# Performance work log

Hardware: AMD Instinct MI355X
Metric: run time of the kernel (lower is better)

## Reference

```python
import jax, jax.numpy as jnp
import numpy as np

D_MODEL = 1024
N_EXPERTS = 8
TOP_K = 2


def setup_inputs() -> dict:
    key = jax.random.key(0)
    ks = jax.random.split(key, 8)
    B, S, D, E, H = 4, 2048, D_MODEL, N_EXPERTS, 4 * D_MODEL
    s1 = 1.0 / np.sqrt(D)
    s2 = 1.0 / np.sqrt(H)
    return {
        "x": jax.random.normal(ks[0], (B, S, D), dtype=jnp.float32),
        "Wg": jax.random.uniform(ks[1], (D, E), jnp.float32, -s1, s1),
        "bg": jax.random.uniform(ks[2], (E,), jnp.float32, -s1, s1),
        "W1": jax.random.uniform(ks[3], (E, D, H), jnp.float32, -s1, s1),
        "b1": jax.random.uniform(ks[4], (E, H), jnp.float32, -s1, s1),
        "W2": jax.random.uniform(ks[5], (E, H, D), jnp.float32, -s2, s2),
        "b2": jax.random.uniform(ks[6], (E, D), jnp.float32, -s2, s2),
    }


def reference(x, Wg, bg, W1, b1, W2, b2):
    B, S, D = x.shape
    E = Wg.shape[1]
    x_flat = x.reshape(-1, D)                      # [T, D]
    logits = x_flat @ Wg + bg                      # [T, E]
    weights = jax.nn.softmax(logits, axis=-1)
    topk_w, topk_idx = jax.lax.top_k(weights, TOP_K)  # [T, K]
    # Per-token combine weight for each expert (sum over k where routed).
    onehot = jax.nn.one_hot(topk_idx, E, dtype=x.dtype)      # [T, K, E]
    combine = jnp.einsum("tk,tke->te", topk_w, onehot)       # [T, E]
    out = jnp.zeros_like(x_flat)
    for e in range(E):  # small fixed loop over experts
        h = jax.nn.gelu(x_flat @ W1[e] + b1[e], approximate=False)
        out = out + combine[:, e:e + 1] * (h @ W2[e] + b2[e])
    return out.reshape(B, S, D)
```

## Files before the change

### kernel.cpp

```cpp
#include <hip/hip_runtime.h>
#include <hip/hip_bf16.h>
#include <math.h>

#define T_TOK 8192
#define DM    1024
#define NE    8
#define HD    4096

typedef __bf16 bf16;
typedef __attribute__((ext_vector_type(8))) __bf16 bf16x8;
typedef __attribute__((ext_vector_type(4))) __bf16 bf16x4;
typedef __attribute__((ext_vector_type(4))) float  f32x4;

__device__ __forceinline__ void gl_lds16(const void* g, void* l) {
  __builtin_amdgcn_global_load_lds((const __attribute__((address_space(1))) void*)g,
                                   (__attribute__((address_space(3))) void*)l, 16, 0, 0);
}

__device__ __forceinline__ int imin(int a, int b) { return a < b ? a : b; }

__global__ void zero_kernel(float* __restrict__ out, int* __restrict__ counts) {
  size_t stride = (size_t)gridDim.x * blockDim.x;
  size_t n4 = (size_t)T_TOK * DM / 4;
  for (size_t i = (size_t)blockIdx.x * blockDim.x + threadIdx.x; i < n4; i += stride) {
    float4 z = {0.f, 0.f, 0.f, 0.f};
    ((float4*)out)[i] = z;
  }
  if (blockIdx.x == 0 && threadIdx.x < NE) counts[threadIdx.x] = 0;
}

__global__ void cvt_x_kernel(const float* __restrict__ x, bf16* __restrict__ xb) {
  size_t stride = (size_t)gridDim.x * blockDim.x;
  size_t n4 = (size_t)T_TOK * DM / 4;
  for (size_t i = (size_t)blockIdx.x * blockDim.x + threadIdx.x; i < n4; i += stride) {
    float4 v = ((const float4*)x)[i];
    bf16x4 o;
    o[0] = (bf16)v.x; o[1] = (bf16)v.y; o[2] = (bf16)v.z; o[3] = (bf16)v.w;
    *(bf16x4*)(xb + 4 * i) = o;
  }
}

__global__ void transpose_cvt_kernel(const float* __restrict__ in, bf16* __restrict__ out,
                                     int R, int C) {
  __shared__ float tile[32][33];
  int e = blockIdx.z;
  int c0 = blockIdx.x * 32, r0 = blockIdx.y * 32;
  int tx = threadIdx.x & 31, ty = threadIdx.x >> 5;
#pragma unroll
  for (int j = 0; j < 4; ++j)
    tile[ty + 8 * j][tx] = in[((size_t)e * R + (r0 + ty + 8 * j)) * C + (c0 + tx)];
  __syncthreads();
#pragma unroll
  for (int j = 0; j < 4; ++j)
    out[((size_t)e * C + (c0 + ty + 8 * j)) * R + (r0 + tx)] = (bf16)tile[tx][ty + 8 * j];
}

__global__ void gating_kernel(const float* __restrict__ x, const float* __restrict__ Wg,
                              const float* __restrict__ bg, int* __restrict__ counts,
                              int* __restrict__ tokl, float* __restrict__ wgt) {
  int t = blockIdx.x * 4 + (threadIdx.x >> 6);
  int lane = threadIdx.x & 63;
  if (t >= T_TOK) return;
  double acc[NE];
#pragma unroll
  for (int e = 0; e < NE; ++e) acc[e] = 0.0;
  const float* xr = x + (size_t)t * DM;
  for (int d = lane; d < DM; d += 64) {
    float xv = xr[d];
#pragma unroll
    for (int e = 0; e < NE; ++e) acc[e] += (double)xv * (double)Wg[d * NE + e];
  }
#pragma unroll
  for (int e = 0; e < NE; ++e)
    for (int o = 32; o > 0; o >>= 1) acc[e] += __shfl_down(acc[e], o, 64);
  if (lane == 0) {
    float l[NE], w[NE];
    float m = -1e30f;
#pragma unroll
    for (int e = 0; e < NE; ++e) { l[e] = (float)acc[e] + bg[e]; m = fmaxf(m, l[e]); }
    float s = 0.f;
#pragma unroll
    for (int e = 0; e < NE; ++e) { w[e] = expf(l[e] - m); s += w[e]; }
    float inv = 1.f / s;
#pragma unroll
    for (int e = 0; e < NE; ++e) w[e] *= inv;
    int e1 = 0; float v1 = w[0];
#pragma unroll
    for (int e = 1; e < NE; ++e) if (w[e] > v1) { v1 = w[e]; e1 = e; }
    int e2 = -1; float v2 = -1.f;
#pragma unroll
    for (int e = 0; e < NE; ++e) if (e != e1 && w[e] > v2) { v2 = w[e]; e2 = e; }
    int s1 = atomicAdd(&counts[e1], 1);
    tokl[e1 * T_TOK + s1] = t; wgt[e1 * T_TOK + s1] = v1;
    int s2 = atomicAdd(&counts[e2], 1);
    tokl[e2 * T_TOK + s2] = t; wgt[e2 * T_TOK + s2] = v2;
  }
}

__global__ void scan_kernel(const int* __restrict__ counts, int* __restrict__ offsets) {
  if (threadIdx.x == 0 && blockIdx.x == 0) {
    int s = 0;
#pragma unroll
    for (int e = 0; e < NE; ++e) { offsets[e] = s; s += counts[e]; }
    offsets[NE] = s;
  }
}

__global__ __launch_bounds__(256) void gemm1_kernel(
    const bf16* __restrict__ xbf, const bf16* __restrict__ w1t,
    const float* __restrict__ b1, const int* __restrict__ counts,
    const int* __restrict__ offsets, const int* __restrict__ tokl,
    bf16* __restrict__ hbuf, int Hc, int cbase) {
  int bid = blockIdx.x;
  int e = bid % NE;
  int pe = bid / NE;
  int NT = Hc / 128;
  int nt = pe % NT, rt = pe / NT;
  int cnt = counts[e];
  if (rt * 128 >= cnt) return;
  __shared__ __align__(16) bf16 sA[128 * 32];
  __shared__ __align__(16) bf16 sB[128 * 32];
  int tid = threadIdx.x, lane = tid & 63, w = tid >> 6;
  int slot0 = w * 2048 + lane * 16;
  int ra0 = slot0 >> 6, ko0 = slot0 & 63;
  int ra1 = ra0 + 16, ko1 = ko0;
  int hoff = offsets[e];
  int r0 = imin(rt * 128 + ra0, cnt - 1);
  int r1 = imin(rt * 128 + ra1, cnt - 1);
  int t0 = tokl[e * T_TOK + r0];
  int t1 = tokl[e * T_TOK + r1];
  const char* ga0 = (const char*)(xbf + (size_t)t0 * DM) + ko0;
  const char* ga1 = (const char*)(xbf + (size_t)t1 * DM) + ko1;
  const char* gb0 = (const char*)(w1t + ((size_t)e * HD + cbase + nt * 128 + ra0) * DM) + ko0;
  const char* gb1 = (const char*)(w1t + ((size_t)e * HD + cbase + nt * 128 + ra1) * DM) + ko1;
  char* la = (char*)sA + w * 2048;
  char* lb = (char*)sB + w * 2048;
  f32x4 acc[4][4];
#pragma unroll
  for (int i = 0; i < 4; ++i)
#pragma unroll
    for (int j = 0; j < 4; ++j) acc[i][j] = {0.f, 0.f, 0.f, 0.f};
  int mw = (w & 1) * 64, nw = (w >> 1) * 64;
  const bf16* pa = sA + (size_t)(mw + (lane & 15)) * 32 + (lane >> 4) * 8;
  const bf16* pb = sB + (size_t)(nw + (lane & 15)) * 32 + (lane >> 4) * 8;
  for (int kk = 0; kk < DM; kk += 32) {
    gl_lds16(ga0 + kk * 2, la);
    gl_lds16(ga1 + kk * 2, la + 1024);
    gl_lds16(gb0 + kk * 2, lb);
    gl_lds16(gb1 + kk * 2, lb + 1024);
    __syncthreads();
    bf16x8 af[4], bfr[4];
#pragma unroll
    for (int i = 0; i < 4; ++i) af[i] = *(const bf16x8*)(pa + i * 16 * 32);
#pragma unroll
    for (int j = 0; j < 4; ++j) bfr[j] = *(const bf16x8*)(pb + j * 16 * 32);
#pragma unroll
    for (int i = 0; i < 4; ++i)
#pragma unroll
      for (int j = 0; j < 4; ++j)
        acc[i][j] = __builtin_amdgcn_mfma_f32_16x16x32_bf16(af[i], bfr[j], acc[i][j], 0, 0, 0);
    __syncthreads();
  }
  int colq = lane & 15, rowq = (lane >> 4) * 4;
  float b1v[4];
#pragma unroll
  for (int j = 0; j < 4; ++j)
    b1v[j] = b1[(size_t)e * HD + cbase + nt * 128 + nw + j * 16 + colq];
#pragma unroll
  for (int i = 0; i < 4; ++i) {
#pragma unroll
    for (int r = 0; r < 4; ++r) {
      int row_l = mw + i * 16 + rowq + r;
      int grow = rt * 128 + row_l;
      if (grow < cnt) {
        size_t hrow = (size_t)(hoff + grow) * Hc;
#pragma unroll
        for (int j = 0; j < 4; ++j) {
          float v = acc[i][j][r] + b1v[j];
          float g = 0.5f * v * (1.f + erff(v * 0.70710678118654752f));
          hbuf[hrow + nt * 128 + nw + j * 16 + colq] = (bf16)g;
        }
      }
    }
  }
}

__global__ __launch_bounds__(256) void gemm2_kernel(
    const bf16* __restrict__ hbuf, const bf16* __restrict__ w2t,
    const float* __restrict__ b2, const int* __restrict__ counts,
    const int* __restrict__ offsets, const int* __restrict__ tokl,
    const float* __restrict__ wgt, float* __restrict__ out,
    int Hc, int cbase, float b2scale) {
  int bid = blockIdx.x;
  int e = bid % NE;
  int pe = bid / NE;
  const int NT = DM / 128;
  int nt = pe % NT, rt = pe / NT;
  int cnt = counts[e];
  if (rt * 128 >= cnt) return;
  __shared__ __align__(16) bf16 sA[128 * 32];
  __shared__ __align__(16) bf16 sB[128 * 32];
  int tid = threadIdx.x, lane = tid & 63, w = tid >> 6;
  int slot0 = w * 2048 + lane * 16;
  int ra0 = slot0 >> 6, ko0 = slot0 & 63;
  int ra1 = ra0 + 16, ko1 = ko0;
  int hoff = offsets[e];
  int r0 = imin(rt * 128 + ra0, cnt - 1);
  int r1 = imin(rt * 128 + ra1, cnt - 1);
  const char* ga0 = (const char*)(hbuf + (size_t)(hoff + r0) * Hc) + ko0;
  const char* ga1 = (const char*)(hbuf + (size_t)(hoff + r1) * Hc) + ko1;
  const char* gb0 = (const char*)(w2t + ((size_t)e * DM + nt * 128 + ra0) * HD + cbase) + ko0;
  const char* gb1 = (const char*)(w2t + ((size_t)e * DM + nt * 128 + ra1) * HD + cbase) + ko1;
  char* la = (char*)sA + w * 2048;
  char* lb = (char*)sB + w * 2048;
  f32x4 acc[4][4];
#pragma unroll
  for (int i = 0; i < 4; ++i)
#pragma unroll
    for (int j = 0; j < 4; ++j) acc[i][j] = {0.f, 0.f, 0.f, 0.f};
  int mw = (w & 1) * 64, nw = (w >> 1) * 64;
  const bf16* pa = sA + (size_t)(mw + (lane & 15)) * 32 + (lane >> 4) * 8;
  const bf16* pb = sB + (size_t)(nw + (lane & 15)) * 32 + (lane >> 4) * 8;
  for (int kk = 0; kk < Hc; kk += 32) {
    gl_lds16(ga0 + kk * 2, la);
    gl_lds16(ga1 + kk * 2, la + 1024);
    gl_lds16(gb0 + kk * 2, lb);
    gl_lds16(gb1 + kk * 2, lb + 1024);
    __syncthreads();
    bf16x8 af[4], bfr[4];
#pragma unroll
    for (int i = 0; i < 4; ++i) af[i] = *(const bf16x8*)(pa + i * 16 * 32);
#pragma unroll
    for (int j = 0; j < 4; ++j) bfr[j] = *(const bf16x8*)(pb + j * 16 * 32);
#pragma unroll
    for (int i = 0; i < 4; ++i)
#pragma unroll
      for (int j = 0; j < 4; ++j)
        acc[i][j] = __builtin_amdgcn_mfma_f32_16x16x32_bf16(af[i], bfr[j], acc[i][j], 0, 0, 0);
    __syncthreads();
  }
  int colq = lane & 15, rowq = (lane >> 4) * 4;
  float b2v[4];
#pragma unroll
  for (int j = 0; j < 4; ++j)
    b2v[j] = b2[(size_t)e * DM + nt * 128 + nw + j * 16 + colq] * b2scale;
#pragma unroll
  for (int i = 0; i < 4; ++i) {
#pragma unroll
    for (int r = 0; r < 4; ++r) {
      int row_l = mw + i * 16 + rowq + r;
      int grow = rt * 128 + row_l;
      if (grow < cnt) {
        float wv = wgt[e * T_TOK + grow];
        int tk = tokl[e * T_TOK + grow];
        float* orow = out + (size_t)tk * DM + nt * 128 + nw;
#pragma unroll
        for (int j = 0; j < 4; ++j)
          atomicAdd(orow + j * 16 + colq, wv * (acc[i][j][r] + b2v[j]));
      }
    }
  }
}

extern "C" void kernel_launch(void* const* d_in, const int* in_sizes, int n_in,
                              void* d_out, int out_size, void* d_ws, size_t ws_size,
                              hipStream_t stream) {
  const float* x  = (const float*)d_in[0];
  const float* Wg = (const float*)d_in[1];
  const float* bg = (const float*)d_in[2];
  const float* W1 = (const float*)d_in[3];
  const float* b1 = (const float*)d_in[4];
  const float* W2 = (const float*)d_in[5];
  const float* b2 = (const float*)d_in[6];
  float* out = (float*)d_out;

  char* ws = (char*)d_ws;
  size_t off = 0;
  auto alloc = [&](size_t bytes) -> void* {
    void* p = ws + off;
    off = (off + bytes + 255) & ~(size_t)255;
    return p;
  };
  int*   counts  = (int*)alloc(NE * 4);
  int*   offsets = (int*)alloc((NE + 1) * 4);
  int*   tokl    = (int*)alloc((size_t)NE * T_TOK * 4);
  float* wgt     = (float*)alloc((size_t)NE * T_TOK * 4);
  bf16*  xbf     = (bf16*)alloc((size_t)T_TOK * DM * 2);
  bf16*  w1t     = (bf16*)alloc((size_t)NE * HD * DM * 2);
  bf16*  w2t     = (bf16*)alloc((size_t)NE * DM * HD * 2);
  size_t remain = ws_size > off ? ws_size - off : 0;
  int Hc = HD;
  while (Hc > 128 && (size_t)2 * T_TOK * Hc * 2 > remain) Hc >>= 1;
  bf16* hbuf = (bf16*)alloc((size_t)2 * T_TOK * Hc * 2);

  zero_kernel<<<4096, 256, 0, stream>>>(out, counts);
  cvt_x_kernel<<<2048, 256, 0, stream>>>(x, xbf);
  transpose_cvt_kernel<<<dim3(HD / 32, DM / 32, NE), 256, 0, stream>>>(W1, w1t, DM, HD);
  transpose_cvt_kernel<<<dim3(DM / 32, HD / 32, NE), 256, 0, stream>>>(W2, w2t, HD, DM);
  gating_kernel<<<T_TOK / 4, 256, 0, stream>>>(x, Wg, bg, counts, tokl, wgt);
  scan_kernel<<<1, 64, 0, stream>>>(counts, offsets);

  int nchunk = HD / Hc;
  for (int c = 0; c < nchunk; ++c) {
    gemm1_kernel<<<NE * (Hc / 128) * (T_TOK / 128), 256, 0, stream>>>(
        xbf, w1t, b1, counts, offsets, tokl, hbuf, Hc, c * Hc);
    gemm2_kernel<<<NE * (DM / 128) * (T_TOK / 128), 256, 0, stream>>>(
        hbuf, w2t, b2, counts, offsets, tokl, wgt, out, Hc, c * Hc, c == 0 ? 1.f : 0.f);
  }
}
```

Baseline: 1.028 ms.

## Widen expert GEMM tiles to 128x256 and vectorize weight transpose

Both expert GEMM kernels now use a 128x256 output tile, with each wave computing 64x128 through 4x8 MFMA accumulators. This roughly halves how often the activation tile is reloaded and doubles the MFMA work per LDS A-fragment read. Launch bounds request 2 blocks per CU to keep the extra accumulator registers under control. The weight transpose-and-convert kernel moves to 64x64 tiles with float4 loads and 16-byte bf16x8 stores. The risks are higher register pressure, fewer blocks per expert, which can reduce parallelism for small expert counts, and more LDS per block.

```diff
diff --git a/kernel.cpp b/kernel.cpp
--- a/kernel.cpp
+++ b/kernel.cpp
@@ -42,17 +42,31 @@
 
 __global__ void transpose_cvt_kernel(const float* __restrict__ in, bf16* __restrict__ out,
                                      int R, int C) {
-  __shared__ float tile[32][33];
+  __shared__ float tile[64][65];
   int e = blockIdx.z;
-  int c0 = blockIdx.x * 32, r0 = blockIdx.y * 32;
-  int tx = threadIdx.x & 31, ty = threadIdx.x >> 5;
-#pragma unroll
-  for (int j = 0; j < 4; ++j)
-    tile[ty + 8 * j][tx] = in[((size_t)e * R + (r0 + ty + 8 * j)) * C + (c0 + tx)];
+  int c0 = blockIdx.x * 64, r0 = blockIdx.y * 64;
+  int tid = threadIdx.x;
+  int lr = tid >> 2, lc = (tid & 3) * 16;
+  const float* src = in + ((size_t)e * R + r0 + lr) * C + c0 + lc;
+#pragma unroll
+  for (int q = 0; q < 4; ++q) {
+    float4 v = *(const float4*)(src + q * 4);
+    tile[lr][lc + q * 4 + 0] = v.x;
+    tile[lr][lc + q * 4 + 1] = v.y;
+    tile[lr][lc + q * 4 + 2] = v.z;
+    tile[lr][lc + q * 4 + 3] = v.w;
+  }
   __syncthreads();
-#pragma unroll
-  for (int j = 0; j < 4; ++j)
-    out[((size_t)e * C + (c0 + ty + 8 * j)) * R + (r0 + tx)] = (bf16)tile[tx][ty + 8 * j];
+  int oc = tid >> 3;
+  int rchunk = tid & 7;
+#pragma unroll
+  for (int q = 0; q < 2; ++q) {
+    int ocq = oc + q * 32;
+    bf16x8 o;
+#pragma unroll
+    for (int k = 0; k < 8; ++k) o[k] = (bf16)tile[rchunk * 8 + k][ocq];
+    *(bf16x8*)(out + ((size_t)e * C + c0 + ocq) * R + r0 + rchunk * 8) = o;
+  }
 }
 
 __global__ void gating_kernel(const float* __restrict__ x, const float* __restrict__ Wg,
@@ -106,7 +120,7 @@
   }
 }
 
-__global__ __launch_bounds__(256) void gemm1_kernel(
+__global__ __launch_bounds__(256, 2) void gemm1_kernel(
     const bf16* __restrict__ xbf, const bf16* __restrict__ w1t,
     const float* __restrict__ b1, const int* __restrict__ counts,
     const int* __restrict__ offsets, const int* __restrict__ tokl,
@@ -114,78 +128,80 @@
   int bid = blockIdx.x;
   int e = bid % NE;
   int pe = bid / NE;
-  int NT = Hc / 128;
+  int NT = Hc / 256;
   int nt = pe % NT, rt = pe / NT;
   int cnt = counts[e];
   if (rt * 128 >= cnt) return;
   __shared__ __align__(16) bf16 sA[128 * 32];
-  __shared__ __align__(16) bf16 sB[128 * 32];
+  __shared__ __align__(16) bf16 sB[256 * 32];
   int tid = threadIdx.x, lane = tid & 63, w = tid >> 6;
-  int slot0 = w * 2048 + lane * 16;
-  int ra0 = slot0 >> 6, ko0 = slot0 & 63;
-  int ra1 = ra0 + 16, ko1 = ko0;
+  int slotA = w * 2048 + lane * 16;
+  int raw0 = slotA >> 6, ko = slotA & 63;
   int hoff = offsets[e];
-  int r0 = imin(rt * 128 + ra0, cnt - 1);
-  int r1 = imin(rt * 128 + ra1, cnt - 1);
+  int r0 = imin(rt * 128 + raw0, cnt - 1);
+  int r1 = imin(rt * 128 + raw0 + 16, cnt - 1);
   int t0 = tokl[e * T_TOK + r0];
   int t1 = tokl[e * T_TOK + r1];
-  const char* ga0 = (const char*)(xbf + (size_t)t0 * DM) + ko0;
-  const char* ga1 = (const char*)(xbf + (size_t)t1 * DM) + ko1;
-  const char* gb0 = (const char*)(w1t + ((size_t)e * HD + cbase + nt * 128 + ra0) * DM) + ko0;
-  const char* gb1 = (const char*)(w1t + ((size_t)e * HD + cbase + nt * 128 + ra1) * DM) + ko1;
+  const char* ga0 = (const char*)(xbf + (size_t)t0 * DM) + ko;
+  const char* ga1 = (const char*)(xbf + (size_t)t1 * DM) + ko;
+  const char* gb[4];
+#pragma unroll
+  for (int c = 0; c < 4; ++c) {
+    int rb = (w * 4096 + c * 1024 + lane * 16) >> 6;
+    gb[c] = (const char*)(w1t + ((size_t)e * HD + cbase + nt * 256 + rb) * DM) + ko;
+  }
   char* la = (char*)sA + w * 2048;
-  char* lb = (char*)sB + w * 2048;
-  f32x4 acc[4][4];
+  char* lb = (char*)sB + w * 4096;
+  f32x4 acc[4][8];
 #pragma unroll
   for (int i = 0; i < 4; ++i)
 #pragma unroll
-    for (int j = 0; j < 4; ++j) acc[i][j] = {0.f, 0.f, 0.f, 0.f};
-  int mw = (w & 1) * 64, nw = (w >> 1) * 64;
+    for (int j = 0; j < 8; ++j) acc[i][j] = {0.f, 0.f, 0.f, 0.f};
+  int mw = (w & 1) * 64, nwv = (w >> 1) * 128;
   const bf16* pa = sA + (size_t)(mw + (lane & 15)) * 32 + (lane >> 4) * 8;
-  const bf16* pb = sB + (size_t)(nw + (lane & 15)) * 32 + (lane >> 4) * 8;
+  const bf16* pb = sB + (size_t)(nwv + (lane & 15)) * 32 + (lane >> 4) * 8;
   for (int kk = 0; kk < DM; kk += 32) {
     gl_lds16(ga0 + kk * 2, la);
     gl_lds16(ga1 + kk * 2, la + 1024);
-    gl_lds16(gb0 + kk * 2, lb);
-    gl_lds16(gb1 + kk * 2, lb + 1024);
+#pragma unroll
+    for (int c = 0; c < 4; ++c) gl_lds16(gb[c] + kk * 2, lb + c * 1024);
     __syncthreads();
-    bf16x8 af[4], bfr[4];
+    bf16x8 af[4], bfr[8];
 #pragma unroll
     for (int i = 0; i < 4; ++i) af[i] = *(const bf16x8*)(pa + i * 16 * 32);
 #pragma unroll
-    for (int j = 0; j < 4; ++j) bfr[j] = *(const bf16x8*)(pb + j * 16 * 32);
+    for (int j = 0; j < 8; ++j) bfr[j] = *(const bf16x8*)(pb + j * 16 * 32);
 #pragma unroll
     for (int i = 0; i < 4; ++i)
 #pragma unroll
-      for (int j = 0; j < 4; ++j)
+      for (int j = 0; j < 8; ++j)
         acc[i][j] = __builtin_amdgcn_mfma_f32_16x16x32_bf16(af[i], bfr[j], acc[i][j], 0, 0, 0);
     __syncthreads();
   }
   int colq = lane & 15, rowq = (lane >> 4) * 4;
-  float b1v[4];
-#pragma unroll
-  for (int j = 0; j < 4; ++j)
-    b1v[j] = b1[(size_t)e * HD + cbase + nt * 128 + nw + j * 16 + colq];
+  float b1v[8];
+#pragma unroll
+  for (int j = 0; j < 8; ++j)
+    b1v[j] = b1[(size_t)e * HD + cbase + nt * 256 + nwv + j * 16 + colq];
 #pragma unroll
   for (int i = 0; i < 4; ++i) {
 #pragma unroll
     for (int r = 0; r < 4; ++r) {
-      int row_l = mw + i * 16 + rowq + r;
-      int grow = rt * 128 + row_l;
+      int grow = rt * 128 + mw + i * 16 + rowq + r;
       if (grow < cnt) {
         size_t hrow = (size_t)(hoff + grow) * Hc;
 #pragma unroll
-        for (int j = 0; j < 4; ++j) {
+        for (int j = 0; j < 8; ++j) {
           float v = acc[i][j][r] + b1v[j];
           float g = 0.5f * v * (1.f + erff(v * 0.70710678118654752f));
-          hbuf[hrow + nt * 128 + nw + j * 16 + colq] = (bf16)g;
+          hbuf[hrow + nt * 256 + nwv + j * 16 + colq] = (bf16)g;
         }
       }
     }
   }
 }
 
-__global__ __launch_bounds__(256) void gemm2_kernel(
+__global__ __launch_bounds__(256, 2) void gemm2_kernel(
     const bf16* __restrict__ hbuf, const bf16* __restrict__ w2t,
     const float* __restrict__ b2, const int* __restrict__ counts,
     const int* __restrict__ offsets, const int* __restrict__ tokl,
@@ -194,68 +210,70 @@
   int bid = blockIdx.x;
   int e = bid % NE;
   int pe = bid / NE;
-  const int NT = DM / 128;
+  const int NT = DM / 256;
   int nt = pe % NT, rt = pe / NT;
   int cnt = counts[e];
   if (rt * 128 >= cnt) return;
   __shared__ __align__(16) bf16 sA[128 * 32];
-  __shared__ __align__(16) bf16 sB[128 * 32];
+  __shared__ __align__(16) bf16 sB[256 * 32];
   int tid = threadIdx.x, lane = tid & 63, w = tid >> 6;
-  int slot0 = w * 2048 + lane * 16;
-  int ra0 = slot0 >> 6, ko0 = slot0 & 63;
-  int ra1 = ra0 + 16, ko1 = ko0;
+  int slotA = w * 2048 + lane * 16;
+  int raw0 = slotA >> 6, ko = slotA & 63;
   int hoff = offsets[e];
-  int r0 = imin(rt * 128 + ra0, cnt - 1);
-  int r1 = imin(rt * 128 + ra1, cnt - 1);
-  const char* ga0 = (const char*)(hbuf + (size_t)(hoff + r0) * Hc) + ko0;
-  const char* ga1 = (const char*)(hbuf + (size_t)(hoff + r1) * Hc) + ko1;
-  const char* gb0 = (const char*)(w2t + ((size_t)e * DM + nt * 128 + ra0) * HD + cbase) + ko0;
-  const char* gb1 = (const char*)(w2t + ((size_t)e * DM + nt * 128 + ra1) * HD + cbase) + ko1;
+  int r0 = imin(rt * 128 + raw0, cnt - 1);
+  int r1 = imin(rt * 128 + raw0 + 16, cnt - 1);
+  const char* ga0 = (const char*)(hbuf + (size_t)(hoff + r0) * Hc) + ko;
+  const char* ga1 = (const char*)(hbuf + (size_t)(hoff + r1) * Hc) + ko;
+  const char* gb[4];
+#pragma unroll
+  for (int c = 0; c < 4; ++c) {
+    int rb = (w * 4096 + c * 1024 + lane * 16) >> 6;
+    gb[c] = (const char*)(w2t + ((size_t)e * DM + nt * 256 + rb) * HD + cbase) + ko;
+  }
   char* la = (char*)sA + w * 2048;
-  char* lb = (char*)sB + w * 2048;
-  f32x4 acc[4][4];
+  char* lb = (char*)sB + w * 4096;
+  f32x4 acc[4][8];
 #pragma unroll
   for (int i = 0; i < 4; ++i)
 #pragma unroll
-    for (int j = 0; j < 4; ++j) acc[i][j] = {0.f, 0.f, 0.f, 0.f};
-  int mw = (w & 1) * 64, nw = (w >> 1) * 64;
+    for (int j = 0; j < 8; ++j) acc[i][j] = {0.f, 0.f, 0.f, 0.f};
+  int mw = (w & 1) * 64, nwv = (w >> 1) * 128;
   const bf16* pa = sA + (size_t)(mw + (lane & 15)) * 32 + (lane >> 4) * 8;
-  const bf16* pb = sB + (size_t)(nw + (lane & 15)) * 32 + (lane >> 4) * 8;
+  const bf16* pb = sB + (size_t)(nwv + (lane & 15)) * 32 + (lane >> 4) * 8;
   for (int kk = 0; kk < Hc; kk += 32) {
     gl_lds16(ga0 + kk * 2, la);
     gl_lds16(ga1 + kk * 2, la + 1024);
-    gl_lds16(gb0 + kk * 2, lb);
-    gl_lds16(gb1 + kk * 2, lb + 1024);
+#pragma unroll
+    for (int c = 0; c < 4; ++c) gl_lds16(gb[c] + kk * 2, lb + c * 1024);
     __syncthreads();
-    bf16x8 af[4], bfr[4];
+    bf16x8 af[4], bfr[8];
 #pragma unroll
     for (int i = 0; i < 4; ++i) af[i] = *(const bf16x8*)(pa + i * 16 * 32);
 #pragma unroll
-    for (int j = 0; j < 4; ++j) bfr[j] = *(const bf16x8*)(pb + j * 16 * 32);
+    for (int j = 0; j < 8; ++j) bfr[j] = *(const bf16x8*)(pb + j * 16 * 32);
 #pragma unroll
     for (int i = 0; i < 4; ++i)
 #pragma unroll
-      for (int j = 0; j < 4; ++j)
+      for (int j = 0; j < 8; ++j)
         acc[i][j] = __builtin_amdgcn_mfma_f32_16x16x32_bf16(af[i], bfr[j], acc[i][j], 0, 0, 0);
     __syncthreads();
   }
   int colq = lane & 15, rowq = (lane >> 4) * 4;
-  float b2v[4];
-#pragma unroll
-  for (int j = 0; j < 4; ++j)
-    b2v[j] = b2[(size_t)e * DM + nt * 128 + nw + j * 16 + colq] * b2scale;
+  float b2v[8];
+#pragma unroll
+  for (int j = 0; j < 8; ++j)
+    b2v[j] = b2[(size_t)e * DM + nt * 256 + nwv + j * 16 + colq] * b2scale;
 #pragma unroll
   for (int i = 0; i < 4; ++i) {
 #pragma unroll
     for (int r = 0; r < 4; ++r) {
-      int row_l = mw + i * 16 + rowq + r;
-      int grow = rt * 128 + row_l;
+      int grow = rt * 128 + mw + i * 16 + rowq + r;
       if (grow < cnt) {
         float wv = wgt[e * T_TOK + grow];
         int tk = tokl[e * T_TOK + grow];
-        float* orow = out + (size_t)tk * DM + nt * 128 + nw;
-#pragma unroll
-        for (int j = 0; j < 4; ++j)
+        float* orow = out + (size_t)tk * DM + nt * 256 + nwv;
+#pragma unroll
+        for (int j = 0; j < 8; ++j)
           atomicAdd(orow + j * 16 + colq, wv * (acc[i][j][r] + b2v[j]));
       }
     }
@@ -290,21 +308,21 @@
   bf16*  w2t     = (bf16*)alloc((size_t)NE * DM * HD * 2);
   size_t remain = ws_size > off ? ws_size - off : 0;
   int Hc = HD;
-  while (Hc > 128 && (size_t)2 * T_TOK * Hc * 2 > remain) Hc >>= 1;
+  while (Hc > 256 && (size_t)2 * T_TOK * Hc * 2 > remain) Hc >>= 1;
   bf16* hbuf = (bf16*)alloc((size_t)2 * T_TOK * Hc * 2);
 
   zero_kernel<<<4096, 256, 0, stream>>>(out, counts);
   cvt_x_kernel<<<2048, 256, 0, stream>>>(x, xbf);
-  transpose_cvt_kernel<<<dim3(HD / 32, DM / 32, NE), 256, 0, stream>>>(W1, w1t, DM, HD);
-  transpose_cvt_kernel<<<dim3(DM / 32, HD / 32, NE), 256, 0, stream>>>(W2, w2t, HD, DM);
+  transpose_cvt_kernel<<<dim3(HD / 64, DM / 64, NE), 256, 0, stream>>>(W1, w1t, DM, HD);
+  transpose_cvt_kernel<<<dim3(DM / 64, HD / 64, NE), 256, 0, stream>>>(W2, w2t, HD, DM);
   gating_kernel<<<T_TOK / 4, 256, 0, stream>>>(x, Wg, bg, counts, tokl, wgt);
   scan_kernel<<<1, 64, 0, stream>>>(counts, offsets);
 
   int nchunk = HD / Hc;
   for (int c = 0; c < nchunk; ++c) {
-    gemm1_kernel<<<NE * (Hc / 128) * (T_TOK / 128), 256, 0, stream>>>(
+    gemm1_kernel<<<NE * (Hc / 256) * (T_TOK / 128), 256, 0, stream>>>(
         xbf, w1t, b1, counts, offsets, tokl, hbuf, Hc, c * Hc);
-    gemm2_kernel<<<NE * (DM / 128) * (T_TOK / 128), 256, 0, stream>>>(
+    gemm2_kernel<<<NE * (DM / 256) * (T_TOK / 128), 256, 0, stream>>>(
         hbuf, w2t, b2, counts, offsets, tokl, wgt, out, Hc, c * Hc, c == 0 ? 1.f : 0.f);
   }
 }
```

After: 1.118 ms. 1.09x slower.

## Double-buffer LDS in expert GEMMs and vectorize weight transpose

Applied to the files above, without the earlier changes.

Both expert GEMM kernels now keep two LDS buffers and issue the next K-slice's global-to-LDS loads before computing the current one. A partial vmcnt wait plus raw barriers replaces the full __syncthreads, so load latency can overlap MFMA work. Launch bounds ask for 3 blocks per CU. The weight transpose/convert kernel uses 64x64 tiles with float4 loads and 16-byte bf16 stores, cutting memory transactions in preprocessing. The hand-written waitcnt and barrier sequence is fragile, and doubling LDS per block may limit occupancy.

```diff
diff --git a/kernel.cpp b/kernel.cpp
--- a/kernel.cpp
+++ b/kernel.cpp
@@ -16,6 +16,9 @@
   __builtin_amdgcn_global_load_lds((const __attribute__((address_space(1))) void*)g,
                                    (__attribute__((address_space(3))) void*)l, 16, 0, 0);
 }
+
+#define RAW_BARRIER() asm volatile("s_barrier" ::: "memory")
+#define WAIT_VM4()    asm volatile("s_waitcnt vmcnt(4)" ::: "memory")
 
 __device__ __forceinline__ int imin(int a, int b) { return a < b ? a : b; }
 
@@ -42,17 +45,31 @@
 
 __global__ void transpose_cvt_kernel(const float* __restrict__ in, bf16* __restrict__ out,
                                      int R, int C) {
-  __shared__ float tile[32][33];
+  __shared__ float tile[64][65];
   int e = blockIdx.z;
-  int c0 = blockIdx.x * 32, r0 = blockIdx.y * 32;
-  int tx = threadIdx.x & 31, ty = threadIdx.x >> 5;
-#pragma unroll
-  for (int j = 0; j < 4; ++j)
-    tile[ty + 8 * j][tx] = in[((size_t)e * R + (r0 + ty + 8 * j)) * C + (c0 + tx)];
+  int c0 = blockIdx.x * 64, r0 = blockIdx.y * 64;
+  int tid = threadIdx.x;
+  int lr = tid >> 2, lc = (tid & 3) * 16;
+  const float* src = in + ((size_t)e * R + r0 + lr) * C + c0 + lc;
+#pragma unroll
+  for (int q = 0; q < 4; ++q) {
+    float4 v = *(const float4*)(src + q * 4);
+    tile[lr][lc + q * 4 + 0] = v.x;
+    tile[lr][lc + q * 4 + 1] = v.y;
+    tile[lr][lc + q * 4 + 2] = v.z;
+    tile[lr][lc + q * 4 + 3] = v.w;
+  }
   __syncthreads();
-#pragma unroll
-  for (int j = 0; j < 4; ++j)
-    out[((size_t)e * C + (c0 + ty + 8 * j)) * R + (r0 + tx)] = (bf16)tile[tx][ty + 8 * j];
+  int oc = tid >> 3;
+  int rchunk = tid & 7;
+#pragma unroll
+  for (int q = 0; q < 2; ++q) {
+    int ocq = oc + q * 32;
+    bf16x8 o;
+#pragma unroll
+    for (int k = 0; k < 8; ++k) o[k] = (bf16)tile[rchunk * 8 + k][ocq];
+    *(bf16x8*)(out + ((size_t)e * C + c0 + ocq) * R + r0 + rchunk * 8) = o;
+  }
 }
 
 __global__ void gating_kernel(const float* __restrict__ x, const float* __restrict__ Wg,
@@ -106,7 +123,7 @@
   }
 }
 
-__global__ __launch_bounds__(256) void gemm1_kernel(
+__global__ __launch_bounds__(256, 3) void gemm1_kernel(
     const bf16* __restrict__ xbf, const bf16* __restrict__ w1t,
     const float* __restrict__ b1, const int* __restrict__ counts,
     const int* __restrict__ offsets, const int* __restrict__ tokl,
@@ -118,48 +135,56 @@
   int nt = pe % NT, rt = pe / NT;
   int cnt = counts[e];
   if (rt * 128 >= cnt) return;
-  __shared__ __align__(16) bf16 sA[128 * 32];
-  __shared__ __align__(16) bf16 sB[128 * 32];
+  __shared__ __align__(16) bf16 sA[2][128 * 32];
+  __shared__ __align__(16) bf16 sB[2][128 * 32];
   int tid = threadIdx.x, lane = tid & 63, w = tid >> 6;
-  int slot0 = w * 2048 + lane * 16;
-  int ra0 = slot0 >> 6, ko0 = slot0 & 63;
-  int ra1 = ra0 + 16, ko1 = ko0;
+  int slot = w * 2048 + lane * 16;
+  int ra0 = slot >> 6, ko = slot & 63;
   int hoff = offsets[e];
   int r0 = imin(rt * 128 + ra0, cnt - 1);
-  int r1 = imin(rt * 128 + ra1, cnt - 1);
+  int r1 = imin(rt * 128 + ra0 + 16, cnt - 1);
   int t0 = tokl[e * T_TOK + r0];
   int t1 = tokl[e * T_TOK + r1];
-  const char* ga0 = (const char*)(xbf + (size_t)t0 * DM) + ko0;
-  const char* ga1 = (const char*)(xbf + (size_t)t1 * DM) + ko1;
-  const char* gb0 = (const char*)(w1t + ((size_t)e * HD + cbase + nt * 128 + ra0) * DM) + ko0;
-  const char* gb1 = (const char*)(w1t + ((size_t)e * HD + cbase + nt * 128 + ra1) * DM) + ko1;
-  char* la = (char*)sA + w * 2048;
-  char* lb = (char*)sB + w * 2048;
+  const char* ga0 = (const char*)(xbf + (size_t)t0 * DM) + ko;
+  const char* ga1 = (const char*)(xbf + (size_t)t1 * DM) + ko;
+  const char* gb0 = (const char*)(w1t + ((size_t)e * HD + cbase + nt * 128 + ra0) * DM) + ko;
+  const char* gb1 = (const char*)(w1t + ((size_t)e * HD + cbase + nt * 128 + ra0 + 16) * DM) + ko;
+  char* lab = (char*)sA + w * 2048;
+  char* lbb = (char*)sB + w * 2048;
   f32x4 acc[4][4];
 #pragma unroll
   for (int i = 0; i < 4; ++i)
 #pragma unroll
     for (int j = 0; j < 4; ++j) acc[i][j] = {0.f, 0.f, 0.f, 0.f};
   int mw = (w & 1) * 64, nw = (w >> 1) * 64;
-  const bf16* pa = sA + (size_t)(mw + (lane & 15)) * 32 + (lane >> 4) * 8;
-  const bf16* pb = sB + (size_t)(nw + (lane & 15)) * 32 + (lane >> 4) * 8;
-  for (int kk = 0; kk < DM; kk += 32) {
-    gl_lds16(ga0 + kk * 2, la);
-    gl_lds16(ga1 + kk * 2, la + 1024);
-    gl_lds16(gb0 + kk * 2, lb);
-    gl_lds16(gb1 + kk * 2, lb + 1024);
-    __syncthreads();
+  const bf16* pa = &sA[0][0] + (size_t)(mw + (lane & 15)) * 32 + (lane >> 4) * 8;
+  const bf16* pb = &sB[0][0] + (size_t)(nw + (lane & 15)) * 32 + (lane >> 4) * 8;
+  const int K = DM / 32;
+  gl_lds16(ga0, lab);
+  gl_lds16(ga1, lab + 1024);
+  gl_lds16(gb0, lbb);
+  gl_lds16(gb1, lbb + 1024);
+  for (int k = 0; k < K; ++k) {
+    int nb = (k + 1) & 1;
+    int kb = (k + 1 < K) ? (k + 1) * 64 : 0;
+    gl_lds16(ga0 + kb, lab + nb * 8192);
+    gl_lds16(ga1 + kb, lab + nb * 8192 + 1024);
+    gl_lds16(gb0 + kb, lbb + nb * 8192);
+    gl_lds16(gb1 + kb, lbb + nb * 8192 + 1024);
+    WAIT_VM4();
+    RAW_BARRIER();
+    int cb = (k & 1) * 4096;
     bf16x8 af[4], bfr[4];
 #pragma unroll
-    for (int i = 0; i < 4; ++i) af[i] = *(const bf16x8*)(pa + i * 16 * 32);
-#pragma unroll
-    for (int j = 0; j < 4; ++j) bfr[j] = *(const bf16x8*)(pb + j * 16 * 32);
+    for (int i = 0; i < 4; ++i) af[i] = *(const bf16x8*)(pa + cb + i * 16 * 32);
+#pragma unroll
+    for (int j = 0; j < 4; ++j) bfr[j] = *(const bf16x8*)(pb + cb + j * 16 * 32);
 #pragma unroll
     for (int i = 0; i < 4; ++i)
 #pragma unroll
       for (int j = 0; j < 4; ++j)
         acc[i][j] = __builtin_amdgcn_mfma_f32_16x16x32_bf16(af[i], bfr[j], acc[i][j], 0, 0, 0);
-    __syncthreads();
+    RAW_BARRIER();
   }
   int colq = lane & 15, rowq = (lane >> 4) * 4;
   float b1v[4];
@@ -170,8 +195,7 @@
   for (int i = 0; i < 4; ++i) {
 #pragma unroll
     for (int r = 0; r < 4; ++r) {
-      int row_l = mw + i * 16 + rowq + r;
-      int grow = rt * 128 + row_l;
+      int grow = rt * 128 + mw + i * 16 + rowq + r;
       if (grow < cnt) {
         size_t hrow = (size_t)(hoff + grow) * Hc;
 #pragma unroll
@@ -185,7 +209,7 @@
   }
 }
 
-__global__ __launch_bounds__(256) void gemm2_kernel(
+__global__ __launch_bounds__(256, 3) void gemm2_kernel(
     const bf16* __restrict__ hbuf, const bf16* __restrict__ w2t,
     const float* __restrict__ b2, const int* __restrict__ counts,
     const int* __restrict__ offsets, const int* __restrict__ tokl,
@@ -198,46 +222,54 @@
   int nt = pe % NT, rt = pe / NT;
   int cnt = counts[e];
   if (rt * 128 >= cnt) return;
-  __shared__ __align__(16) bf16 sA[128 * 32];
-  __shared__ __align__(16) bf16 sB[128 * 32];
+  __shared__ __align__(16) bf16 sA[2][128 * 32];
+  __shared__ __align__(16) bf16 sB[2][128 * 32];
   int tid = threadIdx.x, lane = tid & 63, w = tid >> 6;
-  int slot0 = w * 2048 + lane * 16;
-  int ra0 = slot0 >> 6, ko0 = slot0 & 63;
-  int ra1 = ra0 + 16, ko1 = ko0;
+  int slot = w * 2048 + lane * 16;
+  int ra0 = slot >> 6, ko = slot & 63;
   int hoff = offsets[e];
   int r0 = imin(rt * 128 + ra0, cnt - 1);
-  int r1 = imin(rt * 128 + ra1, cnt - 1);
-  const char* ga0 = (const char*)(hbuf + (size_t)(hoff + r0) * Hc) + ko0;
-  const char* ga1 = (const char*)(hbuf + (size_t)(hoff + r1) * Hc) + ko1;
-  const char* gb0 = (const char*)(w2t + ((size_t)e * DM + nt * 128 + ra0) * HD + cbase) + ko0;
-  const char* gb1 = (const char*)(w2t + ((size_t)e * DM + nt * 128 + ra1) * HD + cbase) + ko1;
-  char* la = (char*)sA + w * 2048;
-  char* lb = (char*)sB + w * 2048;
+  int r1 = imin(rt * 128 + ra0 + 16, cnt - 1);
+  const char* ga0 = (const char*)(hbuf + (size_t)(hoff + r0) * Hc) + ko;
+  const char* ga1 = (const char*)(hbuf + (size_t)(hoff + r1) * Hc) + ko;
+  const char* gb0 = (const char*)(w2t + ((size_t)e * DM + nt * 128 + ra0) * HD + cbase) + ko;
+  const char* gb1 = (const char*)(w2t + ((size_t)e * DM + nt * 128 + ra0 + 16) * HD + cbase) + ko;
+  char* lab = (char*)sA + w * 2048;
+  char* lbb = (char*)sB + w * 2048;
   f32x4 acc[4][4];
 #pragma unroll
   for (int i = 0; i < 4; ++i)
 #pragma unroll
     for (int j = 0; j < 4; ++j) acc[i][j] = {0.f, 0.f, 0.f, 0.f};
   int mw = (w & 1) * 64, nw = (w >> 1) * 64;
-  const bf16* pa = sA + (size_t)(mw + (lane & 15)) * 32 + (lane >> 4) * 8;
-  const bf16* pb = sB + (size_t)(nw + (lane & 15)) * 32 + (lane >> 4) * 8;
-  for (int kk = 0; kk < Hc; kk += 32) {
-    gl_lds16(ga0 + kk * 2, la);
-    gl_lds16(ga1 + kk * 2, la + 1024);
-    gl_lds16(gb0 + kk * 2, lb);
-    gl_lds16(gb1 + kk * 2, lb + 1024);
-    __syncthreads();
+  const bf16* pa = &sA[0][0] + (size_t)(mw + (lane & 15)) * 32 + (lane >> 4) * 8;
+  const bf16* pb = &sB[0][0] + (size_t)(nw + (lane & 15)) * 32 + (lane >> 4) * 8;
+  const int K = Hc / 32;
+  gl_lds16(ga0, lab);
+  gl_lds16(ga1, lab + 1024);
+  gl_lds16(gb0, lbb);
+  gl_lds16(gb1, lbb + 1024);
+  for (int k = 0; k < K; ++k) {
+    int nb = (k + 1) & 1;
+    int kb = (k + 1 < K) ? (k + 1) * 64 : 0;
+    gl_lds16(ga0 + kb, lab + nb * 8192);
+    gl_lds16(ga1 + kb, lab + nb * 8192 + 1024);
+    gl_lds16(gb0 + kb, lbb + nb * 8192);
+    gl_lds16(gb1 + kb, lbb + nb * 8192 + 1024);
+    WAIT_VM4();
+    RAW_BARRIER();
+    int cb = (k & 1) * 4096;
     bf16x8 af[4], bfr[4];
 #pragma unroll
-    for (int i = 0; i < 4; ++i) af[i] = *(const bf16x8*)(pa + i * 16 * 32);
-#pragma unroll
-    for (int j = 0; j < 4; ++j) bfr[j] = *(const bf16x8*)(pb + j * 16 * 32);
+    for (int i = 0; i < 4; ++i) af[i] = *(const bf16x8*)(pa + cb + i * 16 * 32);
+#pragma unroll
+    for (int j = 0; j < 4; ++j) bfr[j] = *(const bf16x8*)(pb + cb + j * 16 * 32);
 #pragma unroll
     for (int i = 0; i < 4; ++i)
 #pragma unroll
       for (int j = 0; j < 4; ++j)
         acc[i][j] = __builtin_amdgcn_mfma_f32_16x16x32_bf16(af[i], bfr[j], acc[i][j], 0, 0, 0);
-    __syncthreads();
+    RAW_BARRIER();
   }
   int colq = lane & 15, rowq = (lane >> 4) * 4;
   float b2v[4];
@@ -248,8 +280,7 @@
   for (int i = 0; i < 4; ++i) {
 #pragma unroll
     for (int r = 0; r < 4; ++r) {
-      int row_l = mw + i * 16 + rowq + r;
-      int grow = rt * 128 + row_l;
+      int grow = rt * 128 + mw + i * 16 + rowq + r;
       if (grow < cnt) {
         float wv = wgt[e * T_TOK + grow];
         int tk = tokl[e * T_TOK + grow];
@@ -295,8 +326,8 @@
 
   zero_kernel<<<4096, 256, 0, stream>>>(out, counts);
   cvt_x_kernel<<<2048, 256, 0, stream>>>(x, xbf);
-  transpose_cvt_kernel<<<dim3(HD / 32, DM / 32, NE), 256, 0, stream>>>(W1, w1t, DM, HD);
-  transpose_cvt_kernel<<<dim3(DM / 32, HD / 32, NE), 256, 0, stream>>>(W2, w2t, HD, DM);
+  transpose_cvt_kernel<<<dim3(HD / 64, DM / 64, NE), 256, 0, stream>>>(W1, w1t, DM, HD);
+  transpose_cvt_kernel<<<dim3(DM / 64, HD / 64, NE), 256, 0, stream>>>(W2, w2t, HD, DM);
   gating_kernel<<<T_TOK / 4, 256, 0, stream>>>(x, Wg, bg, counts, tokl, wgt);
   scan_kernel<<<1, 64, 0, stream>>>(counts, offsets);
 
```

Measured after the change: 1.008 ms. Within noise of the previous version (-1.9%).
